# Kernel tuning notes

Hardware: AMD Instinct MI355X
Metric: run time of the kernel (lower is better)

## Reference

```python
import jax, jax.numpy as jnp
import numpy as np

H, D = 16, 1024
HD = D // H  # 64

def setup_inputs() -> dict:
    key = jax.random.key(0)
    ks = jax.random.split(key, 11)
    B, S = 2, 2048
    s_in = 1.0 / np.sqrt(D)
    return {
        "V": jax.random.normal(ks[0], (B, S, D), jnp.float32),
        "K": jax.random.normal(ks[1], (B, S, D), jnp.float32),
        "Q": jax.random.normal(ks[2], (B, S, D), jnp.float32),
        # stacked per-head Linear weights, torch layout [out,in] -> [H, HD, D]
        "Wv": jax.random.normal(ks[3], (H, HD, D), jnp.float32) * s_in,
        "bv": jnp.zeros((H, HD), jnp.float32),
        "Wk": jax.random.normal(ks[4], (H, HD, D), jnp.float32) * s_in,
        "bk": jnp.zeros((H, HD), jnp.float32),
        "Wq": jax.random.normal(ks[5], (H, HD, D), jnp.float32) * s_in,
        "bq": jnp.zeros((H, HD), jnp.float32),
        "Wo": jax.random.normal(ks[6], (D, D), jnp.float32) * s_in,
        "bo": jnp.zeros((D,), jnp.float32),
    }

def reference(V, K, Q, Wv, bv, Wk, bk, Wq, bq, Wo, bo):
    scale = HD ** (-0.5)
    # per-head projections fused into one batched GEMM: [B,S,D] x [H,HD,D] -> [B,H,S,HD]
    q = jnp.einsum('bsd,hed->bhse', Q, Wq) + bq[None, :, None, :]
    k = jnp.einsum('bsd,hed->bhse', K, Wk) + bk[None, :, None, :]
    v = jnp.einsum('bsd,hed->bhse', V, Wv) + bv[None, :, None, :]
    # scaled dot-product attention
    scores = jnp.einsum('bhqe,bhke->bhqk', q, k) * scale  # [B,H,S,S]
    p = jax.nn.softmax(scores, axis=-1)
    att = jnp.einsum('bhqk,bhke->bhqe', p, v)  # [B,H,S,HD]
    # concat heads (head 0 first, matching the torch cat order) then output proj
    B, _, S, _ = att.shape
    cat = jnp.transpose(att, (0, 2, 1, 3)).reshape(B, S, H * HD)
    return cat @ Wo.T + bo
```

## Files before the change

### kernel.cpp

```cpp
#include <hip/hip_runtime.h>
#include <cstdint>
#include <cstddef>

typedef __bf16 bf16_t;
typedef bf16_t bf16x8 __attribute__((ext_vector_type(8)));
typedef bf16_t bf16x4 __attribute__((ext_vector_type(4)));
typedef float f32x4 __attribute__((ext_vector_type(4)));

__device__ __forceinline__ void gl_lds16(const void* g, void* l) {
  __builtin_amdgcn_global_load_lds(
      (const __attribute__((address_space(1))) void*)g,
      (__attribute__((address_space(3))) void*)l, 16, 0, 0);
}

__device__ __forceinline__ f32x4 mfma16(bf16x8 a, bf16x8 b, f32x4 c) {
  return __builtin_amdgcn_mfma_f32_16x16x32_bf16(a, b, c, 0, 0, 0);
}

struct CvtWArgs { const float* src[4]; };

__global__ __launch_bounds__(256) void convert_w(CvtWArgs a, bf16_t* __restrict__ dst) {
  unsigned g = blockIdx.x * 256u + threadIdx.x;
  unsigned seg = g >> 17, off = g & 0x1FFFFu;
  const float4* s = (const float4*)a.src[seg] + (size_t)off * 2;
  float4 x0 = s[0], x1 = s[1];
  bf16x8 o;
  o[0] = (bf16_t)x0.x; o[1] = (bf16_t)x0.y; o[2] = (bf16_t)x0.z; o[3] = (bf16_t)x0.w;
  o[4] = (bf16_t)x1.x; o[5] = (bf16_t)x1.y; o[6] = (bf16_t)x1.z; o[7] = (bf16_t)x1.w;
  *(bf16x8*)(dst + (size_t)g * 8) = o;
}

struct ProjArgs {
  const float* A[3]; const bf16_t* W[3]; const float* bias[3];
  bf16_t* out[3]; float scale[3];
};

__global__ __launch_bounds__(256, 3) void gemm_proj(ProjArgs p) {
  __shared__ __attribute__((aligned(16))) unsigned char smem[36864];
  bf16_t* a_s = (bf16_t*)smem;
  bf16_t* b_s = (bf16_t*)(smem + 16384);
  const int K = 1024;
  const int z = blockIdx.z;
  const float*  A = p.A[z] + (size_t)blockIdx.x * 128 * K;
  const bf16_t* W = p.W[z] + (size_t)blockIdx.y * 128 * K;

  const int t = threadIdx.x;
  const int w = t >> 6, l = t & 63;
  const int lq = l >> 4, lr = l & 15;
  const int mq = w & 1, nq = w >> 1;

  f32x4 acc[4][4];
  f32x4 zero = {0.f, 0.f, 0.f, 0.f};
  #pragma unroll
  for (int i = 0; i < 4; i++)
    #pragma unroll
    for (int j = 0; j < 4; j++) acc[i][j] = zero;

  for (int k0 = 0; k0 < K; k0 += 64) {
    __syncthreads();
    float4 av[8];
    #pragma unroll
    for (int f = 0; f < 8; f++) {
      int g = t + f * 256;
      int r = g >> 4, c16 = g & 15;
      av[f] = *(const float4*)(A + (size_t)r * K + k0 + c16 * 4);
    }
    #pragma unroll
    for (int i = 0; i < 4; i++) {
      int g = t + i * 256;
      int r = g >> 3, pc = g & 7;
      int lc = pc ^ (r & 7);
      gl_lds16(W + (size_t)r * K + k0 + lc * 8, b_s + i * 2048 + w * 512);
    }
    #pragma unroll
    for (int f = 0; f < 8; f++) {
      int g = t + f * 256;
      int r = g >> 4, c16 = g & 15;
      int phys = (c16 >> 1) ^ (r & 7);
      bf16x4 bv;
      bv[0] = (bf16_t)av[f].x; bv[1] = (bf16_t)av[f].y;
      bv[2] = (bf16_t)av[f].z; bv[3] = (bf16_t)av[f].w;
      *(bf16x4*)(a_s + r * 64 + phys * 8 + (c16 & 1) * 4) = bv;
    }
    __syncthreads();
    #pragma unroll
    for (int kk = 0; kk < 2; kk++) {
      bf16x8 af[4], bfr[4];
      #pragma unroll
      for (int i = 0; i < 4; i++) {
        int R = mq * 64 + i * 16 + lr;
        int ch = (kk * 4 + lq) ^ (R & 7);
        af[i] = *(const bf16x8*)(a_s + R * 64 + ch * 8);
      }
      #pragma unroll
      for (int j = 0; j < 4; j++) {
        int R = nq * 64 + j * 16 + lr;
        int ch = (kk * 4 + lq) ^ (R & 7);
        bfr[j] = *(const bf16x8*)(b_s + R * 64 + ch * 8);
      }
      #pragma unroll
      for (int i = 0; i < 4; i++)
        #pragma unroll
        for (int j = 0; j < 4; j++)
          acc[i][j] = mfma16(af[i], bfr[j], acc[i][j]);
    }
  }

  const float* bias = p.bias[z];
  const float scale = p.scale[z];
  __syncthreads();
  bf16_t* ts = (bf16_t*)smem;
  #pragma unroll
  for (int i = 0; i < 4; i++) {
    #pragma unroll
    for (int j = 0; j < 4; j++) {
      int nl = nq * 64 + j * 16 + lr;
      float bz = bias[blockIdx.y * 128 + nl];
      #pragma unroll
      for (int r = 0; r < 4; r++) {
        int ml = mq * 64 + i * 16 + lq * 4 + r;
        bf16_t val = (bf16_t)((acc[i][j][r] + bz) * scale);
        if (z == 0) {
          int mlp = (ml & 96) | (((ml >> 2) & 3) << 3) | (((ml >> 4) & 1) << 2) | (ml & 3);
          ts[nl * 136 + mlp] = val;
        } else {
          ts[ml * 136 + nl] = val;
        }
      }
    }
  }
  __syncthreads();
  bf16_t* out = p.out[z];
  const int b = blockIdx.x >> 4, sbase = (blockIdx.x & 15) * 128;
  if (z == 0) {
    #pragma unroll
    for (int ii = 0; ii < 8; ii++) {
      int idx = t * 8 + ii * 2048;
      int rr = idx >> 7, cc = idx & 127;
      int n = blockIdx.y * 128 + rr;
      int h = n >> 6, e = n & 63;
      bf16x8 vq = *(const bf16x8*)(ts + rr * 136 + cc);
      *(bf16x8*)(out + ((size_t)(b * 16 + h) * 64 + e) * 2048 + sbase + cc) = vq;
    }
  } else {
    #pragma unroll
    for (int ii = 0; ii < 8; ii++) {
      int idx = t * 8 + ii * 2048;
      int rr = idx >> 7, cc = idx & 127;
      int n = blockIdx.y * 128 + cc;
      int h = n >> 6, e = n & 63;
      bf16x8 vq = *(const bf16x8*)(ts + rr * 136 + cc);
      *(bf16x8*)(out + ((size_t)(b * 16 + h) * 2048 + sbase + rr) * 64 + e) = vq;
    }
  }
}

__global__ __launch_bounds__(256, 4) void attn(
    const bf16_t* __restrict__ qw, const bf16_t* __restrict__ kw,
    const bf16_t* __restrict__ vtw, bf16_t* __restrict__ att)
{
  __shared__ bf16_t k_s[64 * 64];
  __shared__ bf16_t v_s[64 * 64];
  __shared__ bf16_t qe_s[64 * 72];
  const int bh = blockIdx.x, qt = blockIdx.y;
  const int t = threadIdx.x, w = t >> 6, l = t & 63, lq = l >> 4, lr = l & 15;

  const bf16_t* qbase = qw + ((size_t)bh * 2048 + qt * 64) * 64;
  #pragma unroll
  for (int i = 0; i < 2; i++) {
    int g = t + i * 256;
    int r = g >> 3, pc = g & 7;
    int lc = pc ^ (r & 7);
    gl_lds16(qbase + (size_t)r * 64 + lc * 8, qe_s + i * 2048 + w * 512);
  }
  __syncthreads();
  bf16x8 qf[2];
  #pragma unroll
  for (int kk = 0; kk < 2; kk++) {
    int R = w * 16 + lr;
    int ch = (kk * 4 + lq) ^ (R & 7);
    qf[kk] = *(const bf16x8*)(qe_s + R * 64 + ch * 8);
  }

  f32x4 O[4];
  f32x4 zero = {0.f, 0.f, 0.f, 0.f};
  #pragma unroll
  for (int et = 0; et < 4; et++) O[et] = zero;
  float lsum = 0.f;

  for (int kt = 0; kt < 32; ++kt) {
    __syncthreads();
    const bf16_t* kbase = kw + ((size_t)bh * 2048 + kt * 64) * 64;
    const bf16_t* vbase = vtw + (size_t)bh * 131072 + (size_t)kt * 64;
    #pragma unroll
    for (int i = 0; i < 2; i++) {
      int g = t + i * 256;
      int r = g >> 3, pc = g & 7;
      int lc = pc ^ (r & 7);
      gl_lds16(kbase + (size_t)r * 64 + lc * 8, k_s + i * 2048 + w * 512);
      gl_lds16(vbase + (size_t)r * 2048 + lc * 8, v_s + i * 2048 + w * 512);
    }
    __syncthreads();

    f32x4 sc[4];
    #pragma unroll
    for (int j = 0; j < 4; j++) sc[j] = zero;
    #pragma unroll
    for (int kk = 0; kk < 2; kk++) {
      #pragma unroll
      for (int j = 0; j < 4; j++) {
        int R = j * 16 + lr;
        int ch = (kk * 4 + lq) ^ (R & 7);
        bf16x8 kf = *(const bf16x8*)(k_s + R * 64 + ch * 8);
        sc[j] = mfma16(kf, qf[kk], sc[j]);
      }
    }

    bf16x8 pb[2];
    #pragma unroll
    for (int ks2 = 0; ks2 < 2; ks2++) {
      #pragma unroll
      for (int r = 0; r < 4; r++) {
        float e0 = __expf(sc[2 * ks2][r]);
        float e1 = __expf(sc[2 * ks2 + 1][r]);
        lsum += e0 + e1;
        pb[ks2][r] = (bf16_t)e0;
        pb[ks2][4 + r] = (bf16_t)e1;
      }
    }

    #pragma unroll
    for (int ks2 = 0; ks2 < 2; ks2++) {
      #pragma unroll
      for (int et = 0; et < 4; et++) {
        int R = et * 16 + lr;
        int ch = (ks2 * 4 + lq) ^ (R & 7);
        bf16x8 vf = *(const bf16x8*)(v_s + R * 64 + ch * 8);
        O[et] = mfma16(vf, pb[ks2], O[et]);
      }
    }
  }

  float s = lsum;
  s += __shfl_xor(s, 16);
  s += __shfl_xor(s, 32);
  float rinv = 1.0f / s;

  #pragma unroll
  for (int et = 0; et < 4; et++) {
    bf16x4 pv;
    #pragma unroll
    for (int r = 0; r < 4; r++) pv[r] = (bf16_t)(O[et][r] * rinv);
    *(bf16x4*)(qe_s + (w * 16 + lr) * 72 + et * 16 + lq * 4) = pv;
  }
  __syncthreads();
  const int b = bh >> 4, h = bh & 15;
  #pragma unroll
  for (int i = 0; i < 2; i++) {
    int c = t + i * 256;
    int row = c >> 3, c8 = c & 7;
    bf16x8 vv = *(const bf16x8*)(qe_s + row * 72 + c8 * 8);
    *(bf16x8*)(att + ((size_t)b * 2048 + qt * 64 + row) * 1024 + h * 64 + c8 * 8) = vv;
  }
}

__global__ __launch_bounds__(256, 2) void gemm_out(
    const bf16_t* __restrict__ A, const bf16_t* __restrict__ W,
    const float* __restrict__ bias, float* __restrict__ out)
{
  __shared__ bf16_t a_s[64 * 64];
  __shared__ bf16_t b_s[128 * 64];
  const int K = 1024;
  const bf16_t* Ab = A + (size_t)blockIdx.x * 64 * K;
  const bf16_t* Wb = W + (size_t)blockIdx.y * 128 * K;
  const int t = threadIdx.x, w = t >> 6, l = t & 63, lq = l >> 4, lr = l & 15;
  const int mh = w & 1, nh = w >> 1;

  f32x4 acc[2][4];
  f32x4 zero = {0.f, 0.f, 0.f, 0.f};
  #pragma unroll
  for (int i = 0; i < 2; i++)
    #pragma unroll
    for (int j = 0; j < 4; j++) acc[i][j] = zero;

  for (int k0 = 0; k0 < K; k0 += 64) {
    __syncthreads();
    #pragma unroll
    for (int i = 0; i < 2; i++) {
      int g = t + i * 256;
      int r = g >> 3, pc = g & 7;
      int lc = pc ^ (r & 7);
      gl_lds16(Ab + (size_t)r * K + k0 + lc * 8, a_s + i * 2048 + w * 512);
    }
    #pragma unroll
    for (int i = 0; i < 4; i++) {
      int g = t + i * 256;
      int r = g >> 3, pc = g & 7;
      int lc = pc ^ (r & 7);
      gl_lds16(Wb + (size_t)r * K + k0 + lc * 8, b_s + i * 2048 + w * 512);
    }
    __syncthreads();
    #pragma unroll
    for (int kk = 0; kk < 2; kk++) {
      bf16x8 af[2], bfr[4];
      #pragma unroll
      for (int i = 0; i < 2; i++) {
        int R = mh * 32 + i * 16 + lr;
        int ch = (kk * 4 + lq) ^ (R & 7);
        af[i] = *(const bf16x8*)(a_s + R * 64 + ch * 8);
      }
      #pragma unroll
      for (int j = 0; j < 4; j++) {
        int R = nh * 64 + j * 16 + lr;
        int ch = (kk * 4 + lq) ^ (R & 7);
        bfr[j] = *(const bf16x8*)(b_s + R * 64 + ch * 8);
      }
      #pragma unroll
      for (int i = 0; i < 2; i++)
        #pragma unroll
        for (int j = 0; j < 4; j++)
          acc[i][j] = mfma16(af[i], bfr[j], acc[i][j]);
    }
  }

  #pragma unroll
  for (int i = 0; i < 2; i++) {
    #pragma unroll
    for (int j = 0; j < 4; j++) {
      int col = blockIdx.y * 128 + nh * 64 + j * 16 + lr;
      float bz = bias[col];
      #pragma unroll
      for (int r = 0; r < 4; r++) {
        int row = blockIdx.x * 64 + mh * 32 + i * 16 + lq * 4 + r;
        out[(size_t)row * 1024 + col] = acc[i][j][r] + bz;
      }
    }
  }
}

extern "C" void kernel_launch(void* const* d_in, const int* in_sizes, int n_in,
                              void* d_out, int out_size, void* d_ws, size_t ws_size,
                              hipStream_t stream) {
  (void)in_sizes; (void)n_in; (void)out_size;
  const float* V  = (const float*)d_in[0];
  const float* Kx = (const float*)d_in[1];
  const float* Q  = (const float*)d_in[2];
  const float* Wv = (const float*)d_in[3];
  const float* bv = (const float*)d_in[4];
  const float* Wk = (const float*)d_in[5];
  const float* bk = (const float*)d_in[6];
  const float* Wq = (const float*)d_in[7];
  const float* bq = (const float*)d_in[8];
  const float* Wo = (const float*)d_in[9];
  const float* bo = (const float*)d_in[10];

  const size_t E = 1048576;
  if (ws_size < 20 * E * sizeof(bf16_t)) return;

  bf16_t* ws = (bf16_t*)d_ws;
  bf16_t* cWo   = ws;
  bf16_t* cWv   = ws + E;
  bf16_t* cWk   = ws + 2 * E;
  bf16_t* cWq   = ws + 3 * E;
  bf16_t* q_ws  = ws + 4 * E;
  bf16_t* k_ws  = ws + 8 * E;
  bf16_t* vt_ws = ws + 12 * E;
  bf16_t* att_ws= ws + 16 * E;

  CvtWArgs cw;
  cw.src[0] = Wo; cw.src[1] = Wv; cw.src[2] = Wk; cw.src[3] = Wq;
  convert_w<<<2048, 256, 0, stream>>>(cw, ws);

  ProjArgs pa;
  pa.A[0] = V;   pa.A[1] = Kx;  pa.A[2] = Q;
  pa.W[0] = cWv; pa.W[1] = cWk; pa.W[2] = cWq;
  pa.bias[0] = bv; pa.bias[1] = bk; pa.bias[2] = bq;
  pa.out[0] = vt_ws; pa.out[1] = k_ws; pa.out[2] = q_ws;
  pa.scale[0] = 1.f; pa.scale[1] = 1.f; pa.scale[2] = 0.125f;
  gemm_proj<<<dim3(32, 8, 3), 256, 0, stream>>>(pa);

  attn<<<dim3(32, 32), 256, 0, stream>>>(q_ws, k_ws, vt_ws, att_ws);

  gemm_out<<<dim3(64, 8), 256, 0, stream>>>(att_ws, cWo, bo, (float*)d_out);
}
```

Before: 214.7 us.

## Double-buffer LDS tiles in projection and output GEMMs with register prefetch

Both the QKV projection GEMM and the output GEMM now prefetch the next K-tile from global memory into registers while MFMAs run on the current LDS buffer, then write those registers into a second LDS buffer. This drops one barrier per iteration and is meant to hide global-load latency behind compute. In exchange, direct global-to-LDS loads become register-staged loads, LDS use roughly doubles, and the projection kernel's occupancy hint drops from 3 to 2 blocks per CU.

```diff
diff --git a/kernel.cpp b/kernel.cpp
--- a/kernel.cpp
+++ b/kernel.cpp
@@ -35,20 +35,24 @@
   bf16_t* out[3]; float scale[3];
 };
 
-__global__ __launch_bounds__(256, 3) void gemm_proj(ProjArgs p) {
-  __shared__ __attribute__((aligned(16))) unsigned char smem[36864];
-  bf16_t* a_s = (bf16_t*)smem;
-  bf16_t* b_s = (bf16_t*)(smem + 16384);
+__global__ __launch_bounds__(256, 2) void gemm_proj(ProjArgs p) {
+  __shared__ __attribute__((aligned(16))) unsigned char smem[65536];
+  bf16_t* a_buf = (bf16_t*)smem;
+  bf16_t* b_buf = (bf16_t*)(smem + 32768);
   const int K = 1024;
   const int z = blockIdx.z;
   const float*  A = p.A[z] + (size_t)blockIdx.x * 128 * K;
   const bf16_t* W = p.W[z] + (size_t)blockIdx.y * 128 * K;
 
   const int t = threadIdx.x;
-  const int w = t >> 6, l = t & 63;
+  const int l = t & 63;
   const int lq = l >> 4, lr = l & 15;
+  const int w = t >> 6;
   const int mq = w & 1, nq = w >> 1;
 
+  const int ar[8] = { (t + 0*256) >> 4, (t + 1*256) >> 4, (t + 2*256) >> 4, (t + 3*256) >> 4,
+                      (t + 4*256) >> 4, (t + 5*256) >> 4, (t + 6*256) >> 4, (t + 7*256) >> 4 };
+  const int ac16 = t & 15;
   f32x4 acc[4][4];
   f32x4 zero = {0.f, 0.f, 0.f, 0.f};
   #pragma unroll
@@ -56,33 +60,50 @@
     #pragma unroll
     for (int j = 0; j < 4; j++) acc[i][j] = zero;
 
-  for (int k0 = 0; k0 < K; k0 += 64) {
-    __syncthreads();
-    float4 av[8];
+  {
+    float4 av[8]; uint4 wv[4];
+    #pragma unroll
+    for (int f = 0; f < 8; f++)
+      av[f] = *(const float4*)(A + (size_t)ar[f] * K + ac16 * 4);
+    #pragma unroll
+    for (int i = 0; i < 4; i++) {
+      int g = t + i * 256, r = g >> 3, pc = g & 7, lc = pc ^ (r & 7);
+      wv[i] = *(const uint4*)(W + (size_t)r * K + lc * 8);
+    }
     #pragma unroll
     for (int f = 0; f < 8; f++) {
-      int g = t + f * 256;
-      int r = g >> 4, c16 = g & 15;
-      av[f] = *(const float4*)(A + (size_t)r * K + k0 + c16 * 4);
-    }
-    #pragma unroll
-    for (int i = 0; i < 4; i++) {
-      int g = t + i * 256;
-      int r = g >> 3, pc = g & 7;
-      int lc = pc ^ (r & 7);
-      gl_lds16(W + (size_t)r * K + k0 + lc * 8, b_s + i * 2048 + w * 512);
-    }
-    #pragma unroll
-    for (int f = 0; f < 8; f++) {
-      int g = t + f * 256;
-      int r = g >> 4, c16 = g & 15;
-      int phys = (c16 >> 1) ^ (r & 7);
+      int r = ar[f];
+      int phys = (ac16 >> 1) ^ (r & 7);
       bf16x4 bv;
       bv[0] = (bf16_t)av[f].x; bv[1] = (bf16_t)av[f].y;
       bv[2] = (bf16_t)av[f].z; bv[3] = (bf16_t)av[f].w;
-      *(bf16x4*)(a_s + r * 64 + phys * 8 + (c16 & 1) * 4) = bv;
-    }
+      *(bf16x4*)(a_buf + r * 64 + phys * 8 + (ac16 & 1) * 4) = bv;
+    }
+    #pragma unroll
+    for (int i = 0; i < 4; i++) {
+      int g = t + i * 256;
+      *(uint4*)(b_buf + g * 8) = wv[i];
+    }
+  }
+
+  for (int kt = 0; kt < 16; ++kt) {
     __syncthreads();
+    bf16_t* acur = a_buf + (kt & 1) * 8192;
+    bf16_t* bcur = b_buf + (kt & 1) * 8192;
+
+    float4 av[8]; uint4 wv[4];
+    if (kt < 15) {
+      int k0 = (kt + 1) * 64;
+      #pragma unroll
+      for (int f = 0; f < 8; f++)
+        av[f] = *(const float4*)(A + (size_t)ar[f] * K + k0 + ac16 * 4);
+      #pragma unroll
+      for (int i = 0; i < 4; i++) {
+        int g = t + i * 256, r = g >> 3, pc = g & 7, lc = pc ^ (r & 7);
+        wv[i] = *(const uint4*)(W + (size_t)r * K + k0 + lc * 8);
+      }
+    }
+
     #pragma unroll
     for (int kk = 0; kk < 2; kk++) {
       bf16x8 af[4], bfr[4];
@@ -90,19 +111,38 @@
       for (int i = 0; i < 4; i++) {
         int R = mq * 64 + i * 16 + lr;
         int ch = (kk * 4 + lq) ^ (R & 7);
-        af[i] = *(const bf16x8*)(a_s + R * 64 + ch * 8);
+        af[i] = *(const bf16x8*)(acur + R * 64 + ch * 8);
       }
       #pragma unroll
       for (int j = 0; j < 4; j++) {
         int R = nq * 64 + j * 16 + lr;
         int ch = (kk * 4 + lq) ^ (R & 7);
-        bfr[j] = *(const bf16x8*)(b_s + R * 64 + ch * 8);
+        bfr[j] = *(const bf16x8*)(bcur + R * 64 + ch * 8);
       }
       #pragma unroll
       for (int i = 0; i < 4; i++)
         #pragma unroll
         for (int j = 0; j < 4; j++)
           acc[i][j] = mfma16(af[i], bfr[j], acc[i][j]);
+    }
+
+    if (kt < 15) {
+      bf16_t* anx = a_buf + ((kt + 1) & 1) * 8192;
+      bf16_t* bnx = b_buf + ((kt + 1) & 1) * 8192;
+      #pragma unroll
+      for (int f = 0; f < 8; f++) {
+        int r = ar[f];
+        int phys = (ac16 >> 1) ^ (r & 7);
+        bf16x4 bv;
+        bv[0] = (bf16_t)av[f].x; bv[1] = (bf16_t)av[f].y;
+        bv[2] = (bf16_t)av[f].z; bv[3] = (bf16_t)av[f].w;
+        *(bf16x4*)(anx + r * 64 + phys * 8 + (ac16 & 1) * 4) = bv;
+      }
+      #pragma unroll
+      for (int i = 0; i < 4; i++) {
+        int g = t + i * 256;
+        *(uint4*)(bnx + g * 8) = wv[i];
+      }
     }
   }
 
@@ -268,8 +308,9 @@
     const bf16_t* __restrict__ A, const bf16_t* __restrict__ W,
     const float* __restrict__ bias, float* __restrict__ out)
 {
-  __shared__ bf16_t a_s[64 * 64];
-  __shared__ bf16_t b_s[128 * 64];
+  __shared__ __attribute__((aligned(16))) unsigned char smem[49152];
+  bf16_t* a_buf = (bf16_t*)smem;
+  bf16_t* b_buf = (bf16_t*)(smem + 16384);
   const int K = 1024;
   const bf16_t* Ab = A + (size_t)blockIdx.x * 64 * K;
   const bf16_t* Wb = W + (size_t)blockIdx.y * 128 * K;
@@ -283,23 +324,44 @@
     #pragma unroll
     for (int j = 0; j < 4; j++) acc[i][j] = zero;
 
-  for (int k0 = 0; k0 < K; k0 += 64) {
+  {
+    uint4 avv[2], wv[4];
+    #pragma unroll
+    for (int i = 0; i < 2; i++) {
+      int g = t + i * 256, r = g >> 3, pc = g & 7, lc = pc ^ (r & 7);
+      avv[i] = *(const uint4*)(Ab + (size_t)r * K + lc * 8);
+    }
+    #pragma unroll
+    for (int i = 0; i < 4; i++) {
+      int g = t + i * 256, r = g >> 3, pc = g & 7, lc = pc ^ (r & 7);
+      wv[i] = *(const uint4*)(Wb + (size_t)r * K + lc * 8);
+    }
+    #pragma unroll
+    for (int i = 0; i < 2; i++) { int g = t + i * 256; *(uint4*)(a_buf + g * 8) = avv[i]; }
+    #pragma unroll
+    for (int i = 0; i < 4; i++) { int g = t + i * 256; *(uint4*)(b_buf + g * 8) = wv[i]; }
+  }
+
+  for (int kt = 0; kt < 16; ++kt) {
     __syncthreads();
-    #pragma unroll
-    for (int i = 0; i < 2; i++) {
-      int g = t + i * 256;
-      int r = g >> 3, pc = g & 7;
-      int lc = pc ^ (r & 7);
-      gl_lds16(Ab + (size_t)r * K + k0 + lc * 8, a_s + i * 2048 + w * 512);
-    }
-    #pragma unroll
-    for (int i = 0; i < 4; i++) {
-      int g = t + i * 256;
-      int r = g >> 3, pc = g & 7;
-      int lc = pc ^ (r & 7);
-      gl_lds16(Wb + (size_t)r * K + k0 + lc * 8, b_s + i * 2048 + w * 512);
-    }
-    __syncthreads();
+    bf16_t* acur = a_buf + (kt & 1) * 4096;
+    bf16_t* bcur = b_buf + (kt & 1) * 8192;
+
+    uint4 avv[2], wv[4];
+    if (kt < 15) {
+      int k0 = (kt + 1) * 64;
+      #pragma unroll
+      for (int i = 0; i < 2; i++) {
+        int g = t + i * 256, r = g >> 3, pc = g & 7, lc = pc ^ (r & 7);
+        avv[i] = *(const uint4*)(Ab + (size_t)r * K + k0 + lc * 8);
+      }
+      #pragma unroll
+      for (int i = 0; i < 4; i++) {
+        int g = t + i * 256, r = g >> 3, pc = g & 7, lc = pc ^ (r & 7);
+        wv[i] = *(const uint4*)(Wb + (size_t)r * K + k0 + lc * 8);
+      }
+    }
+
     #pragma unroll
     for (int kk = 0; kk < 2; kk++) {
       bf16x8 af[2], bfr[4];
@@ -307,19 +369,28 @@
       for (int i = 0; i < 2; i++) {
         int R = mh * 32 + i * 16 + lr;
         int ch = (kk * 4 + lq) ^ (R & 7);
-        af[i] = *(const bf16x8*)(a_s + R * 64 + ch * 8);
+        af[i] = *(const bf16x8*)(acur + R * 64 + ch * 8);
       }
       #pragma unroll
       for (int j = 0; j < 4; j++) {
         int R = nh * 64 + j * 16 + lr;
         int ch = (kk * 4 + lq) ^ (R & 7);
-        bfr[j] = *(const bf16x8*)(b_s + R * 64 + ch * 8);
+        bfr[j] = *(const bf16x8*)(bcur + R * 64 + ch * 8);
       }
       #pragma unroll
       for (int i = 0; i < 2; i++)
         #pragma unroll
         for (int j = 0; j < 4; j++)
           acc[i][j] = mfma16(af[i], bfr[j], acc[i][j]);
+    }
+
+    if (kt < 15) {
+      bf16_t* anx = a_buf + ((kt + 1) & 1) * 4096;
+      bf16_t* bnx = b_buf + ((kt + 1) & 1) * 8192;
+      #pragma unroll
+      for (int i = 0; i < 2; i++) { int g = t + i * 256; *(uint4*)(anx + g * 8) = avv[i]; }
+      #pragma unroll
+      for (int i = 0; i < 4; i++) { int g = t + i * 256; *(uint4*)(bnx + g * 8) = wv[i]; }
     }
   }
 
```

After: 234.6 us. +9.2%, slower.
